# Kernel optimization log

Hardware: AMD Instinct MI355X
Metric: run time of the kernel (lower is better)

## Reference

```python
import jax, jax.numpy as jnp
import numpy as np


def _lsa(cost):
    """Jonker-Volgenant shortest-augmenting-path LAP (same optimum as
    scipy.optimize.linear_sum_assignment). cost: (n, m) with n <= m.
    Returns col4row: (n,) assigned column for each row."""
    cost = np.asarray(cost, dtype=np.float64)
    n, m = cost.shape
    u = np.zeros(n)
    v = np.zeros(m)
    col4row = np.full(n, -1, dtype=np.int64)
    row4col = np.full(m, -1, dtype=np.int64)
    for cur_row in range(n):
        shortest = np.full(m, np.inf)
        path = np.full(m, -1, dtype=np.int64)
        SR = np.zeros(n, dtype=bool)
        SC = np.zeros(m, dtype=bool)
        i = cur_row
        min_val = 0.0
        sink = -1
        while sink == -1:
            SR[i] = True
            rem = np.where(~SC)[0]
            d = min_val + cost[i, rem] - u[i] - v[rem]
            better = d < shortest[rem]
            shortest[rem[better]] = d[better]
            path[rem[better]] = i
            k = rem[np.argmin(shortest[rem])]
            min_val = shortest[k]
            SC[k] = True
            if row4col[k] == -1:
                sink = k
            else:
                i = row4col[k]
        u[cur_row] += min_val
        upd = SR.copy()
        upd[cur_row] = False
        u[upd] += min_val - shortest[col4row[upd]]
        v[SC] -= min_val - shortest[SC]
        j = sink
        while True:
            i = path[j]
            row4col[j] = i
            col4row[i], j = j, col4row[i]
            if i == cur_row:
                break
    return col4row


def _hungarian(cost_np):
    """Mimic scipy.linear_sum_assignment for any (N, M)."""
    n, m = cost_np.shape
    if n <= m:
        col4row = _lsa(cost_np)
        return np.arange(n, dtype=np.int64), col4row
    else:
        row4col = _lsa(cost_np.T)  # for each col of cost, its assigned row
        return row4col, np.arange(m, dtype=np.int64)


def setup_inputs() -> dict:
    key = jax.random.key(0)
    k1, k2 = jax.random.split(key)
    N, M, P = 1024, 1024, 20
    pred_points = jax.random.normal(k1, (N, P, 2), dtype=jnp.float32)
    gt_points = jax.random.normal(k2, (M, P, 2), dtype=jnp.float32)
    return {"pred_points": pred_points, "gt_points": gt_points}


def reference(pred_points, gt_points):
    N = pred_points.shape[0]
    M = gt_points.shape[0]
    if N == 0 or M == 0:
        return pred_points, jnp.zeros((N, 1), dtype=pred_points.dtype)

    # Fused pairwise cost: mean over points of per-point Euclidean distance.
    diff = pred_points[:, None, :, :] - gt_points[None, :, :, :]  # (N, M, P, 2)
    cost = jnp.sqrt(jnp.sum(diff * diff, axis=-1)).mean(axis=-1)  # (N, M)

    row_ind, col_ind = _hungarian(np.asarray(cost))
    row_ind = jnp.asarray(row_ind)
    col_ind = jnp.asarray(col_ind)

    if N <= M:
        matched = jnp.zeros_like(pred_points)
    else:
        matched = pred_points
    matched = matched.at[row_ind].set(gt_points[col_ind])

    conf = jnp.zeros((N,), dtype=cost.dtype)
    conf = conf.at[row_ind].set(jnp.exp(-cost[row_ind, col_ind]))
    return matched, conf[:, None]
```

## Files before the change

kernel.cpp:

```cpp
#include <hip/hip_runtime.h>
#include <math.h>

#define NN 1024
#define PP 20
#define LPC 16
#define SCALE_D 33554432.0
#define INV_SCALE_F (1.0f / 33554432.0f)
#define IMAX 0x7fffffff
#define ARR_CAP 4096

__device__ __forceinline__ float cost_ij(const float* __restrict__ a,
                                         const float* __restrict__ b) {
#pragma clang fp contract(off)
  float s = 0.0f;
#pragma unroll
  for (int p = 0; p < PP; ++p) {
    float dx = a[2 * p]     - b[2 * p];
    float dy = a[2 * p + 1] - b[2 * p + 1];
    s += sqrtf(dx * dx + dy * dy);
  }
  return s / 20.0f;
}

__global__ void cost_kernel(const float* __restrict__ pred,
                            const float* __restrict__ gt,
                            int* __restrict__ ci) {
  int id = blockIdx.x * blockDim.x + threadIdx.x;
  int i = id >> 10;
  int j = id & (NN - 1);
  float c = cost_ij(pred + i * 40, gt + j * 40);
  ci[id] = (int)((double)c * SCALE_D);
}

__global__ void colmin_kernel(const int* __restrict__ ci,
                              int* __restrict__ colv,
                              int* __restrict__ colr) {
  int j = blockIdx.x * blockDim.x + threadIdx.x;
  int mv = ci[j];
  int mi = 0;
#pragma unroll 8
  for (int i = 1; i < NN; ++i) {
    int c = ci[i * NN + j];
    if (c < mv) { mv = c; mi = i; }
  }
  colv[j] = mv;
  colr[j] = mi;
}

__global__ __launch_bounds__(64) void rowmin_kernel(
    const int* __restrict__ ci, const int* __restrict__ colv,
    int* __restrict__ rm1, int* __restrict__ rm2, int* __restrict__ rj1) {
  const int row = blockIdx.x;
  const int lane = threadIdx.x;
  const int* cr = ci + (size_t)row * NN + lane * LPC;
  const int* vr = colv + lane * LPC;
  int4 ca = ((const int4*)cr)[0], cb = ((const int4*)cr)[1],
       cc = ((const int4*)cr)[2], cd = ((const int4*)cr)[3];
  int4 va = ((const int4*)vr)[0], vb = ((const int4*)vr)[1],
       vc = ((const int4*)vr)[2], vd = ((const int4*)vr)[3];
  int c[LPC] = {ca.x, ca.y, ca.z, ca.w, cb.x, cb.y, cb.z, cb.w,
                cc.x, cc.y, cc.z, cc.w, cd.x, cd.y, cd.z, cd.w};
  int v[LPC] = {va.x, va.y, va.z, va.w, vb.x, vb.y, vb.z, vb.w,
                vc.x, vc.y, vc.z, vc.w, vd.x, vd.y, vd.z, vd.w};
  int m1 = IMAX, m2 = IMAX, c1 = IMAX;
#pragma unroll
  for (int q = 0; q < LPC; ++q) {
    const int d = c[q] - v[q];
    if (d < m1) { m2 = m1; m1 = d; c1 = lane * LPC + q; }
    else if (d < m2) m2 = d;
  }
#pragma unroll
  for (int m = 1; m < 64; m <<= 1) {
    const int pm1 = __shfl_xor(m1, m);
    const int pm2 = __shfl_xor(m2, m);
    const int pc1 = __shfl_xor(c1, m);
    const int hi = (m1 > pm1) ? m1 : pm1;
    const int lo2 = (m2 < pm2) ? m2 : pm2;
    if (pm1 < m1 || (pm1 == m1 && pc1 < c1)) { m1 = pm1; c1 = pc1; }
    m2 = (hi < lo2) ? hi : lo2;
  }
  if (lane == 0) { rm1[row] = m1; rm2[row] = m2; rj1[row] = c1; }
}

__device__ __forceinline__ int wave_min_bcast(int x) {
  int t;
  t = __builtin_amdgcn_update_dpp(IMAX, x, 0x111, 0xf, 0xf, false);
  x = (t < x) ? t : x;
  t = __builtin_amdgcn_update_dpp(IMAX, x, 0x112, 0xf, 0xf, false);
  x = (t < x) ? t : x;
  t = __builtin_amdgcn_update_dpp(IMAX, x, 0x114, 0xf, 0xf, false);
  x = (t < x) ? t : x;
  t = __builtin_amdgcn_update_dpp(IMAX, x, 0x118, 0xf, 0xf, false);
  x = (t < x) ? t : x;
  t = __builtin_amdgcn_update_dpp(IMAX, x, 0x142, 0xf, 0xf, false);
  x = (t < x) ? t : x;
  t = __builtin_amdgcn_update_dpp(IMAX, x, 0x143, 0xf, 0xf, false);
  x = (t < x) ? t : x;
  return __builtin_amdgcn_readlane(x, 63);
}

__global__ __launch_bounds__(64) void lap_kernel(
    const float* __restrict__ gt, const int* __restrict__ ci,
    const int* __restrict__ colv, const int* __restrict__ colr,
    const int* __restrict__ rm1, const int* __restrict__ rm2,
    const int* __restrict__ rj1, float* __restrict__ out) {
  const int lane = threadIdx.x;

  __shared__ int u_s[NN];
  __shared__ int row4col_s[NN];
  __shared__ int col4row_s[NN];
  __shared__ int path_s[NN];
  __shared__ int queue_s[NN + ARR_CAP];

  int nv_r[LPC];
  int sh_r[LPC];
  int kq_r[LPC];
  int pa_r[LPC];
  int rc_r[LPC];

  {
    const int4* p4 = (const int4*)ci;
    int ax = 0, ay = 0, az = 0, aw = 0;
    for (int it = 0; it < (NN * NN / 4) / 64; it += 8) {
#pragma unroll
      for (int uu = 0; uu < 8; ++uu) {
        const int4 tv = p4[(size_t)(it + uu) * 64 + lane];
        ax ^= tv.x; ay ^= tv.y; az ^= tv.z; aw ^= tv.w;
      }
    }
    asm volatile("" :: "v"(ax), "v"(ay), "v"(az), "v"(aw));
  }

#pragma unroll
  for (int q = 0; q < LPC; ++q) {
    const int j = lane * LPC + q;
    u_s[j] = 0;
    row4col_s[j] = -1;
    col4row_s[j] = -1;
  }
  __syncthreads();

  if (lane == 0) {
    for (int j = 0; j < NN; ++j) {
      const int i = colr[j];
      if (col4row_s[i] < 0) { col4row_s[i] = j; row4col_s[j] = i; }
    }
  }
  __syncthreads();

#pragma unroll
  for (int q = 0; q < LPC; ++q) {
    const int j = lane * LPC + q;
    const int i = row4col_s[j];
    int nvv = -colv[j];
    if (i >= 0) {
      const int mu = (rj1[i] == j) ? rm2[i] : rm1[i];
      u_s[i] = mu;
      nvv += mu;
    }
    nv_r[q] = nvv;
  }
  if (lane == 0) {
    int n = 0;
    for (int i = 0; i < NN; ++i)
      if (col4row_s[i] < 0) queue_s[n++] = i;
    path_s[0] = n;
  }
  __syncthreads();
  int head = 0;
  int tail = path_s[0];
  __syncthreads();

  for (int step = 0; step < ARR_CAP && head < tail; ++step) {
    const int i = queue_s[head];
    ++head;
    const int* cr = ci + (size_t)i * NN + lane * LPC;
    int4 ca = ((const int4*)cr)[0], cb = ((const int4*)cr)[1],
         cc = ((const int4*)cr)[2], cd = ((const int4*)cr)[3];
    int c[LPC] = {ca.x, ca.y, ca.z, ca.w, cb.x, cb.y, cb.z, cb.w,
                  cc.x, cc.y, cc.z, cc.w, cd.x, cd.y, cd.z, cd.w};
    int m1 = IMAX, m2 = IMAX, c1 = 0;
#pragma unroll
    for (int q = 0; q < LPC; ++q) {
      const int d = c[q] + nv_r[q];
      if (d < m1) { m2 = m1; m1 = d; c1 = q; }
      else if (d < m2) m2 = d;
    }
    const int m1g = wave_min_bcast(m1);
    const unsigned long long ball = __ballot(m1 == m1g);
    const int wl = __ffsll(ball) - 1;
    const int cand = (lane == wl) ? m2 : m1;
    const int m2g = wave_min_bcast(cand);
    const int j1 = (wl << 4) | __builtin_amdgcn_readlane(c1, wl);
    const int delta = m2g - m1g;
    if (lane == wl && delta > 0) {
#pragma unroll
      for (int q = 0; q < LPC; ++q)
        if (q == (j1 & 15)) nv_r[q] += delta;
    }
    const int k = row4col_s[j1];
    __syncthreads();
    if (lane == 0) {
      u_s[i] = m2g;
      row4col_s[j1] = i;
      col4row_s[i] = j1;
      if (k >= 0) {
        col4row_s[k] = -1;
        queue_s[tail] = k;
      }
    }
    if (k >= 0) ++tail;
    __syncthreads();
  }

#pragma unroll
  for (int q = 0; q < LPC; ++q) rc_r[q] = row4col_s[lane * LPC + q];
  __syncthreads();

  const int nfree = tail - head;
  for (int fi = 0; fi < nfree; ++fi) {
    const int r = queue_s[head + fi];
#pragma unroll
    for (int q = 0; q < LPC; ++q) { sh_r[q] = IMAX; kq_r[q] = IMAX; }
    int i = r;
    int mv = 0;
    int A = __builtin_amdgcn_readfirstlane(-u_s[r]);
    int sink;
    while (true) {
      const int* cr = ci + (size_t)i * NN + lane * LPC;
      int4 ca = ((const int4*)cr)[0], cb = ((const int4*)cr)[1],
           cc = ((const int4*)cr)[2], cd = ((const int4*)cr)[3];
      int c[LPC] = {ca.x, ca.y, ca.z, ca.w, cb.x, cb.y, cb.z, cb.w,
                    cc.x, cc.y, cc.z, cc.w, cd.x, cd.y, cd.z, cd.w};
#pragma unroll
      for (int q = 0; q < LPC; ++q) {
        const int d = A + c[q] + nv_r[q];
        const bool upd = d < sh_r[q];
        sh_r[q] = upd ? d : sh_r[q];
        kq_r[q] = upd ? d : kq_r[q];
        pa_r[q] = upd ? i : pa_r[q];
      }
      int t1k[8], t1e[8], t1r[8];
#pragma unroll
      for (int q = 0; q < 8; ++q) {
        const bool b = kq_r[2 * q + 1] < kq_r[2 * q];
        t1k[q] = b ? kq_r[2 * q + 1] : kq_r[2 * q];
        t1e[q] = b ? 2 * q + 1 : 2 * q;
        t1r[q] = b ? rc_r[2 * q + 1] : rc_r[2 * q];
      }
      int t2k[4], t2e[4], t2r[4];
#pragma unroll
      for (int q = 0; q < 4; ++q) {
        const bool b = t1k[2 * q + 1] < t1k[2 * q];
        t2k[q] = b ? t1k[2 * q + 1] : t1k[2 * q];
        t2e[q] = b ? t1e[2 * q + 1] : t1e[2 * q];
        t2r[q] = b ? t1r[2 * q + 1] : t1r[2 * q];
      }
      int t3k[2], t3e[2], t3r[2];
#pragma unroll
      for (int q = 0; q < 2; ++q) {
        const bool b = t2k[2 * q + 1] < t2k[2 * q];
        t3k[q] = b ? t2k[2 * q + 1] : t2k[2 * q];
        t3e[q] = b ? t2e[2 * q + 1] : t2e[2 * q];
        t3r[q] = b ? t2r[2 * q + 1] : t2r[2 * q];
      }
      const bool b0 = t3k[1] < t3k[0];
      const int bs = b0 ? t3k[1] : t3k[0];
      const int bq = b0 ? t3e[1] : t3e[0];
      const int brc = b0 ? t3r[1] : t3r[0];
      const int minkey = wave_min_bcast(bs);
      const unsigned long long ball = __ballot(bs == minkey);
      const int wl = __ffsll(ball) - 1;
      const int kcol = (wl << 4) | __builtin_amdgcn_readlane(bq, wl);
      const int krc = __builtin_amdgcn_readlane(brc, wl);
      mv = minkey;
      if (krc < 0) { sink = kcol; break; }
      if (lane == (kcol >> 4)) {
#pragma unroll
        for (int q = 0; q < LPC; ++q)
          if (q == (kcol & 15)) kq_r[q] = IMAX;
      }
      i = krc;
      A = __builtin_amdgcn_readfirstlane(mv - u_s[i]);
    }
#pragma unroll
    for (int q = 0; q < LPC; ++q) {
      if (kq_r[q] == IMAX && sh_r[q] != IMAX) {
        const int delta = mv - sh_r[q];
        const int i2 = rc_r[q];
        if (i2 >= 0) u_s[i2] += delta;
        nv_r[q] += delta;
      }
      path_s[lane * LPC + q] = pa_r[q];
    }
    if (lane == 0) u_s[r] += mv;
    __syncthreads();
    if (lane == 0) {
      int j = sink;
      while (true) {
        const int i2 = path_s[j];
        row4col_s[j] = i2;
        const int jn = col4row_s[i2];
        col4row_s[i2] = j;
        j = jn;
        if (i2 == r) break;
      }
    }
    __syncthreads();
#pragma unroll
    for (int q = 0; q < LPC; ++q) rc_r[q] = row4col_s[lane * LPC + q];
  }
  __syncthreads();

#pragma unroll
  for (int q = 0; q < LPC; ++q) {
    const int row = lane * LPC + q;
    const int col = col4row_s[row];
    const float4* g4 = (const float4*)(gt + (size_t)col * 40);
    float4* o4 = (float4*)(out + (size_t)row * 40);
#pragma unroll
    for (int w = 0; w < 10; ++w) o4[w] = g4[w];
    const float cf = (float)ci[(size_t)row * NN + col] * INV_SCALE_F;
    out[NN * 40 + row] = expf(-cf);
  }
}

extern "C" void kernel_launch(void* const* d_in, const int* in_sizes, int n_in,
                              void* d_out, int out_size, void* d_ws,
                              size_t ws_size, hipStream_t stream) {
  const float* pred = (const float*)d_in[0];
  const float* gt = (const float*)d_in[1];
  float* out = (float*)d_out;
  int* ci = (int*)d_ws;

  int* colv = (int*)out;
  int* colr = colv + NN;
  int* rm1 = colr + NN;
  int* rm2 = rm1 + NN;
  int* rj1 = rm2 + NN;

  cost_kernel<<<NN * NN / 256, 256, 0, stream>>>(pred, gt, ci);
  colmin_kernel<<<NN / 256, 256, 0, stream>>>(ci, colv, colr);
  rowmin_kernel<<<NN, 64, 0, stream>>>(ci, colv, rm1, rm2, rj1);
  lap_kernel<<<1, 64, 0, stream>>>(gt, ci, colv, colr, rm1, rm2, rj1, out);
}
```

Baseline: 9.874 ms.

## Prefetch next cost row and fuse argmin payload into DPP reductions

```diff
diff --git a/kernel.cpp b/kernel.cpp
--- a/kernel.cpp
+++ b/kernel.cpp
@@ -82,22 +82,68 @@
   if (lane == 0) { rm1[row] = m1; rm2[row] = m2; rj1[row] = c1; }
 }
 
-__device__ __forceinline__ int wave_min_bcast(int x) {
-  int t;
-  t = __builtin_amdgcn_update_dpp(IMAX, x, 0x111, 0xf, 0xf, false);
-  x = (t < x) ? t : x;
-  t = __builtin_amdgcn_update_dpp(IMAX, x, 0x112, 0xf, 0xf, false);
-  x = (t < x) ? t : x;
-  t = __builtin_amdgcn_update_dpp(IMAX, x, 0x114, 0xf, 0xf, false);
-  x = (t < x) ? t : x;
-  t = __builtin_amdgcn_update_dpp(IMAX, x, 0x118, 0xf, 0xf, false);
-  x = (t < x) ? t : x;
-  t = __builtin_amdgcn_update_dpp(IMAX, x, 0x142, 0xf, 0xf, false);
-  x = (t < x) ? t : x;
-  t = __builtin_amdgcn_update_dpp(IMAX, x, 0x143, 0xf, 0xf, false);
-  x = (t < x) ? t : x;
-  return __builtin_amdgcn_readlane(x, 63);
-}
+template <int CTRL>
+__device__ __forceinline__ void argmin_step(int& k, int& p) {
+  const int k2 = __builtin_amdgcn_update_dpp(IMAX, k, CTRL, 0xf, 0xf, false);
+  const int p2 = __builtin_amdgcn_update_dpp(0, p, CTRL, 0xf, 0xf, false);
+  if (k2 < k) { k = k2; p = p2; }
+}
+__device__ __forceinline__ void wave_argmin(int& k, int& p) {
+  argmin_step<0x111>(k, p);
+  argmin_step<0x112>(k, p);
+  argmin_step<0x114>(k, p);
+  argmin_step<0x118>(k, p);
+  argmin_step<0x142>(k, p);
+  argmin_step<0x143>(k, p);
+}
+template <int CTRL>
+__device__ __forceinline__ void top2_step(int& m1, int& m2, int& p1) {
+  const int a1 = __builtin_amdgcn_update_dpp(IMAX, m1, CTRL, 0xf, 0xf, false);
+  const int a2 = __builtin_amdgcn_update_dpp(IMAX, m2, CTRL, 0xf, 0xf, false);
+  const int ap = __builtin_amdgcn_update_dpp(0, p1, CTRL, 0xf, 0xf, false);
+  const int hi = m1 > a1 ? m1 : a1;
+  const int lo = m2 < a2 ? m2 : a2;
+  if (a1 < m1) { m1 = a1; p1 = ap; }
+  m2 = hi < lo ? hi : lo;
+}
+__device__ __forceinline__ void wave_top2(int& m1, int& m2, int& p1) {
+  top2_step<0x111>(m1, m2, p1);
+  top2_step<0x112>(m1, m2, p1);
+  top2_step<0x114>(m1, m2, p1);
+  top2_step<0x118>(m1, m2, p1);
+  top2_step<0x142>(m1, m2, p1);
+  top2_step<0x143>(m1, m2, p1);
+}
+
+#define LGKM_BARRIER()                                \
+  do {                                                \
+    asm volatile("s_waitcnt lgkmcnt(0)" ::: "memory"); \
+    __builtin_amdgcn_s_barrier();                     \
+  } while (0)
+
+#define PF_ISSUE(row)                                                    \
+  do {                                                                   \
+    const int4* _pr = (const int4*)(ci + (size_t)(row)*NN + lane * LPC); \
+    P0 = _pr[0]; P1 = _pr[1]; P2 = _pr[2]; P3 = _pr[3];                  \
+  } while (0)
+
+#define UNPACK_P(c)                                      \
+  do {                                                   \
+    c[0] = P0.x; c[1] = P0.y; c[2] = P0.z; c[3] = P0.w;  \
+    c[4] = P1.x; c[5] = P1.y; c[6] = P1.z; c[7] = P1.w;  \
+    c[8] = P2.x; c[9] = P2.y; c[10] = P2.z; c[11] = P2.w; \
+    c[12] = P3.x; c[13] = P3.y; c[14] = P3.z; c[15] = P3.w; \
+  } while (0)
+
+#define LOAD_C(c, row)                                                   \
+  do {                                                                   \
+    const int4* _cr = (const int4*)(ci + (size_t)(row)*NN + lane * LPC); \
+    const int4 _a = _cr[0], _b = _cr[1], _d = _cr[2], _e = _cr[3];       \
+    c[0] = _a.x; c[1] = _a.y; c[2] = _a.z; c[3] = _a.w;                  \
+    c[4] = _b.x; c[5] = _b.y; c[6] = _b.z; c[7] = _b.w;                  \
+    c[8] = _d.x; c[9] = _d.y; c[10] = _d.z; c[11] = _d.w;                \
+    c[12] = _e.x; c[13] = _e.y; c[14] = _e.z; c[15] = _e.w;              \
+  } while (0)
 
 __global__ __launch_bounds__(64) void lap_kernel(
     const float* __restrict__ gt, const int* __restrict__ ci,
@@ -116,7 +162,9 @@
   int sh_r[LPC];
   int kq_r[LPC];
   int pa_r[LPC];
-  int rc_r[LPC];
+  int prc_r[LPC];
+  int4 P0, P1, P2, P3;
+  int pf_row = -1;
 
   {
     const int4* p4 = (const int4*)ci;
@@ -171,14 +219,16 @@
   int tail = path_s[0];
   __syncthreads();
 
+  if (head < tail) { pf_row = queue_s[head]; PF_ISSUE(pf_row); }
   for (int step = 0; step < ARR_CAP && head < tail; ++step) {
     const int i = queue_s[head];
     ++head;
-    const int* cr = ci + (size_t)i * NN + lane * LPC;
-    int4 ca = ((const int4*)cr)[0], cb = ((const int4*)cr)[1],
-         cc = ((const int4*)cr)[2], cd = ((const int4*)cr)[3];
-    int c[LPC] = {ca.x, ca.y, ca.z, ca.w, cb.x, cb.y, cb.z, cb.w,
-                  cc.x, cc.y, cc.z, cc.w, cd.x, cd.y, cd.z, cd.w};
+    int c[LPC];
+    if (i == pf_row) { UNPACK_P(c); }
+    else             { LOAD_C(c, i); }
+    if (head < tail) { pf_row = queue_s[head]; PF_ISSUE(pf_row); }
+    else pf_row = -1;
+
     int m1 = IMAX, m2 = IMAX, c1 = 0;
 #pragma unroll
     for (int q = 0; q < LPC; ++q) {
@@ -186,20 +236,19 @@
       if (d < m1) { m2 = m1; m1 = d; c1 = q; }
       else if (d < m2) m2 = d;
     }
-    const int m1g = wave_min_bcast(m1);
-    const unsigned long long ball = __ballot(m1 == m1g);
-    const int wl = __ffsll(ball) - 1;
-    const int cand = (lane == wl) ? m2 : m1;
-    const int m2g = wave_min_bcast(cand);
-    const int j1 = (wl << 4) | __builtin_amdgcn_readlane(c1, wl);
+    int p1 = (lane << 4) | c1;
+    wave_top2(m1, m2, p1);
+    const int m1g = __builtin_amdgcn_readlane(m1, 63);
+    const int m2g = __builtin_amdgcn_readlane(m2, 63);
+    const int j1 = __builtin_amdgcn_readlane(p1, 63);
     const int delta = m2g - m1g;
-    if (lane == wl && delta > 0) {
+    if (lane == (j1 >> 4) && delta > 0) {
 #pragma unroll
       for (int q = 0; q < LPC; ++q)
         if (q == (j1 & 15)) nv_r[q] += delta;
     }
     const int k = row4col_s[j1];
-    __syncthreads();
+    LGKM_BARRIER();
     if (lane == 0) {
       u_s[i] = m2g;
       row4col_s[j1] = i;
@@ -210,14 +259,19 @@
       }
     }
     if (k >= 0) ++tail;
-    __syncthreads();
-  }
-
-#pragma unroll
-  for (int q = 0; q < LPC; ++q) rc_r[q] = row4col_s[lane * LPC + q];
+    LGKM_BARRIER();
+  }
+
+#pragma unroll
+  for (int q = 0; q < LPC; ++q) {
+    const int rcq = row4col_s[lane * LPC + q];
+    prc_r[q] = ((rcq + 1) << 10) | (lane * LPC + q);
+  }
   __syncthreads();
 
   const int nfree = tail - head;
+  pf_row = -1;
+  if (nfree > 0) { pf_row = queue_s[head]; PF_ISSUE(pf_row); }
   for (int fi = 0; fi < nfree; ++fi) {
     const int r = queue_s[head + fi];
 #pragma unroll
@@ -227,11 +281,10 @@
     int A = __builtin_amdgcn_readfirstlane(-u_s[r]);
     int sink;
     while (true) {
-      const int* cr = ci + (size_t)i * NN + lane * LPC;
-      int4 ca = ((const int4*)cr)[0], cb = ((const int4*)cr)[1],
-           cc = ((const int4*)cr)[2], cd = ((const int4*)cr)[3];
-      int c[LPC] = {ca.x, ca.y, ca.z, ca.w, cb.x, cb.y, cb.z, cb.w,
-                    cc.x, cc.y, cc.z, cc.w, cd.x, cd.y, cd.z, cd.w};
+      int c[LPC];
+      if (i == pf_row) { UNPACK_P(c); }
+      else             { LOAD_C(c, i); }
+      pf_row = -1;
 #pragma unroll
       for (int q = 0; q < LPC; ++q) {
         const int d = A + c[q] + nv_r[q];
@@ -240,40 +293,35 @@
         kq_r[q] = upd ? d : kq_r[q];
         pa_r[q] = upd ? i : pa_r[q];
       }
-      int t1k[8], t1e[8], t1r[8];
+      int a1k[8], a1p[8];
 #pragma unroll
       for (int q = 0; q < 8; ++q) {
         const bool b = kq_r[2 * q + 1] < kq_r[2 * q];
-        t1k[q] = b ? kq_r[2 * q + 1] : kq_r[2 * q];
-        t1e[q] = b ? 2 * q + 1 : 2 * q;
-        t1r[q] = b ? rc_r[2 * q + 1] : rc_r[2 * q];
-      }
-      int t2k[4], t2e[4], t2r[4];
+        a1k[q] = b ? kq_r[2 * q + 1] : kq_r[2 * q];
+        a1p[q] = b ? prc_r[2 * q + 1] : prc_r[2 * q];
+      }
+      int a2k[4], a2p[4];
 #pragma unroll
       for (int q = 0; q < 4; ++q) {
-        const bool b = t1k[2 * q + 1] < t1k[2 * q];
-        t2k[q] = b ? t1k[2 * q + 1] : t1k[2 * q];
-        t2e[q] = b ? t1e[2 * q + 1] : t1e[2 * q];
-        t2r[q] = b ? t1r[2 * q + 1] : t1r[2 * q];
-      }
-      int t3k[2], t3e[2], t3r[2];
+        const bool b = a1k[2 * q + 1] < a1k[2 * q];
+        a2k[q] = b ? a1k[2 * q + 1] : a1k[2 * q];
+        a2p[q] = b ? a1p[2 * q + 1] : a1p[2 * q];
+      }
+      int a3k[2], a3p[2];
 #pragma unroll
       for (int q = 0; q < 2; ++q) {
-        const bool b = t2k[2 * q + 1] < t2k[2 * q];
-        t3k[q] = b ? t2k[2 * q + 1] : t2k[2 * q];
-        t3e[q] = b ? t2e[2 * q + 1] : t2e[2 * q];
-        t3r[q] = b ? t2r[2 * q + 1] : t2r[2 * q];
-      }
-      const bool b0 = t3k[1] < t3k[0];
-      const int bs = b0 ? t3k[1] : t3k[0];
-      const int bq = b0 ? t3e[1] : t3e[0];
-      const int brc = b0 ? t3r[1] : t3r[0];
-      const int minkey = wave_min_bcast(bs);
-      const unsigned long long ball = __ballot(bs == minkey);
-      const int wl = __ffsll(ball) - 1;
-      const int kcol = (wl << 4) | __builtin_amdgcn_readlane(bq, wl);
-      const int krc = __builtin_amdgcn_readlane(brc, wl);
-      mv = minkey;
+        const bool b = a2k[2 * q + 1] < a2k[2 * q];
+        a3k[q] = b ? a2k[2 * q + 1] : a2k[2 * q];
+        a3p[q] = b ? a2p[2 * q + 1] : a2p[2 * q];
+      }
+      const bool b0 = a3k[1] < a3k[0];
+      int bk = b0 ? a3k[1] : a3k[0];
+      int bp = b0 ? a3p[1] : a3p[0];
+      wave_argmin(bk, bp);
+      mv = __builtin_amdgcn_readlane(bk, 63);
+      const int pk = __builtin_amdgcn_readlane(bp, 63);
+      const int kcol = pk & 1023;
+      const int krc = (pk >> 10) - 1;
       if (krc < 0) { sink = kcol; break; }
       if (lane == (kcol >> 4)) {
 #pragma unroll
@@ -283,18 +331,19 @@
       i = krc;
       A = __builtin_amdgcn_readfirstlane(mv - u_s[i]);
     }
+    if (fi + 1 < nfree) { pf_row = queue_s[head + fi + 1]; PF_ISSUE(pf_row); }
 #pragma unroll
     for (int q = 0; q < LPC; ++q) {
       if (kq_r[q] == IMAX && sh_r[q] != IMAX) {
         const int delta = mv - sh_r[q];
-        const int i2 = rc_r[q];
+        const int i2 = (prc_r[q] >> 10) - 1;
         if (i2 >= 0) u_s[i2] += delta;
         nv_r[q] += delta;
       }
       path_s[lane * LPC + q] = pa_r[q];
     }
     if (lane == 0) u_s[r] += mv;
-    __syncthreads();
+    LGKM_BARRIER();
     if (lane == 0) {
       int j = sink;
       while (true) {
@@ -306,9 +355,12 @@
         if (i2 == r) break;
       }
     }
-    __syncthreads();
-#pragma unroll
-    for (int q = 0; q < LPC; ++q) rc_r[q] = row4col_s[lane * LPC + q];
+    LGKM_BARRIER();
+#pragma unroll
+    for (int q = 0; q < LPC; ++q) {
+      const int rcq = row4col_s[lane * LPC + q];
+      prc_r[q] = ((rcq + 1) << 10) | (lane * LPC + q);
+    }
   }
   __syncthreads();
 
```

Result: slower. 14.89 ms (+50.8%).

## Add parallel auction-style bidding rounds to pre-assign rows before serial LAP

Applied to the files above, without the earlier changes.

```diff
diff --git a/kernel.cpp b/kernel.cpp
--- a/kernel.cpp
+++ b/kernel.cpp
@@ -7,7 +7,8 @@
 #define SCALE_D 33554432.0
 #define INV_SCALE_F (1.0f / 33554432.0f)
 #define IMAX 0x7fffffff
-#define ARR_CAP 4096
+#define NROUNDS 20
+#define ARR_CAP2 1536
 
 __device__ __forceinline__ float cost_ij(const float* __restrict__ a,
                                          const float* __restrict__ b) {
@@ -32,40 +33,49 @@
   ci[id] = (int)((double)c * SCALE_D);
 }
 
+__global__ void init_kernel(int* __restrict__ u, int* __restrict__ r4c,
+                            int* __restrict__ c4r,
+                            unsigned long long* __restrict__ bids) {
+  const int t = blockIdx.x * blockDim.x + threadIdx.x;
+  u[t] = 0;
+  r4c[t] = -1;
+  c4r[t] = -1;
+  bids[t] = 0ull;
+}
+
 __global__ void colmin_kernel(const int* __restrict__ ci,
-                              int* __restrict__ colv,
-                              int* __restrict__ colr) {
+                              int* __restrict__ v) {
   int j = blockIdx.x * blockDim.x + threadIdx.x;
   int mv = ci[j];
-  int mi = 0;
 #pragma unroll 8
   for (int i = 1; i < NN; ++i) {
     int c = ci[i * NN + j];
-    if (c < mv) { mv = c; mi = i; }
-  }
-  colv[j] = mv;
-  colr[j] = mi;
-}
-
-__global__ __launch_bounds__(64) void rowmin_kernel(
-    const int* __restrict__ ci, const int* __restrict__ colv,
-    int* __restrict__ rm1, int* __restrict__ rm2, int* __restrict__ rj1) {
+    if (c < mv) mv = c;
+  }
+  v[j] = mv;
+}
+
+__global__ __launch_bounds__(64) void bid_kernel(
+    const int* __restrict__ ci, const int* __restrict__ v,
+    const int* __restrict__ c4r, int* __restrict__ bidm2,
+    unsigned long long* __restrict__ bids) {
   const int row = blockIdx.x;
+  if (c4r[row] >= 0) return;
   const int lane = threadIdx.x;
   const int* cr = ci + (size_t)row * NN + lane * LPC;
-  const int* vr = colv + lane * LPC;
+  const int* vr = v + lane * LPC;
   int4 ca = ((const int4*)cr)[0], cb = ((const int4*)cr)[1],
        cc = ((const int4*)cr)[2], cd = ((const int4*)cr)[3];
   int4 va = ((const int4*)vr)[0], vb = ((const int4*)vr)[1],
        vc = ((const int4*)vr)[2], vd = ((const int4*)vr)[3];
   int c[LPC] = {ca.x, ca.y, ca.z, ca.w, cb.x, cb.y, cb.z, cb.w,
                 cc.x, cc.y, cc.z, cc.w, cd.x, cd.y, cd.z, cd.w};
-  int v[LPC] = {va.x, va.y, va.z, va.w, vb.x, vb.y, vb.z, vb.w,
-                vc.x, vc.y, vc.z, vc.w, vd.x, vd.y, vd.z, vd.w};
+  int vv[LPC] = {va.x, va.y, va.z, va.w, vb.x, vb.y, vb.z, vb.w,
+                 vc.x, vc.y, vc.z, vc.w, vd.x, vd.y, vd.z, vd.w};
   int m1 = IMAX, m2 = IMAX, c1 = IMAX;
 #pragma unroll
   for (int q = 0; q < LPC; ++q) {
-    const int d = c[q] - v[q];
+    const int d = c[q] - vv[q];
     if (d < m1) { m2 = m1; m1 = d; c1 = lane * LPC + q; }
     else if (d < m2) m2 = d;
   }
@@ -79,7 +89,32 @@
     if (pm1 < m1 || (pm1 == m1 && pc1 < c1)) { m1 = pm1; c1 = pc1; }
     m2 = (hi < lo2) ? hi : lo2;
   }
-  if (lane == 0) { rm1[row] = m1; rm2[row] = m2; rj1[row] = c1; }
+  if (lane == 0) {
+    bidm2[row] = m2;
+    const unsigned long long pk =
+        ((unsigned long long)(unsigned)(m2 - m1) << 32) |
+        (unsigned long long)(unsigned)(row + 1);
+    atomicMax(&bids[c1], pk);
+  }
+}
+
+__global__ void resolve_kernel(const int* __restrict__ ci, int* __restrict__ v,
+                               int* __restrict__ u, int* __restrict__ r4c,
+                               int* __restrict__ c4r,
+                               const int* __restrict__ bidm2,
+                               unsigned long long* __restrict__ bids) {
+  const int j = blockIdx.x * blockDim.x + threadIdx.x;
+  const unsigned long long b = bids[j];
+  if (b == 0ull) return;
+  bids[j] = 0ull;
+  const int row = (int)(b & 0xffffffffull) - 1;
+  const int m2 = bidm2[row];
+  const int disp = r4c[j];
+  r4c[j] = row;
+  c4r[row] = j;
+  if (disp >= 0) c4r[disp] = -1;
+  v[j] = ci[(size_t)row * NN + j] - m2;
+  u[row] = m2;
 }
 
 __device__ __forceinline__ int wave_min_bcast(int x) {
@@ -101,16 +136,16 @@
 
 __global__ __launch_bounds__(64) void lap_kernel(
     const float* __restrict__ gt, const int* __restrict__ ci,
-    const int* __restrict__ colv, const int* __restrict__ colr,
-    const int* __restrict__ rm1, const int* __restrict__ rm2,
-    const int* __restrict__ rj1, float* __restrict__ out) {
+    const int* __restrict__ v_g, const int* __restrict__ u_g,
+    const int* __restrict__ r4c_g, const int* __restrict__ c4r_g,
+    float* __restrict__ out) {
   const int lane = threadIdx.x;
 
   __shared__ int u_s[NN];
   __shared__ int row4col_s[NN];
   __shared__ int col4row_s[NN];
   __shared__ int path_s[NN];
-  __shared__ int queue_s[NN + ARR_CAP];
+  __shared__ int queue_s[NN + ARR_CAP2];
 
   int nv_r[LPC];
   int sh_r[LPC];
@@ -119,12 +154,13 @@
   int rc_r[LPC];
 
   {
-    const int4* p4 = (const int4*)ci;
+    const char* base = (const char*)ci;
     int ax = 0, ay = 0, az = 0, aw = 0;
-    for (int it = 0; it < (NN * NN / 4) / 64; it += 8) {
+    for (int it = 0; it < 1024; it += 8) {
 #pragma unroll
       for (int uu = 0; uu < 8; ++uu) {
-        const int4 tv = p4[(size_t)(it + uu) * 64 + lane];
+        const int4 tv =
+            *(const int4*)(base + ((size_t)(it + uu) * 64 + lane) * 64);
         ax ^= tv.x; ay ^= tv.y; az ^= tv.z; aw ^= tv.w;
       }
     }
@@ -134,32 +170,12 @@
 #pragma unroll
   for (int q = 0; q < LPC; ++q) {
     const int j = lane * LPC + q;
-    u_s[j] = 0;
-    row4col_s[j] = -1;
-    col4row_s[j] = -1;
-  }
-  __syncthreads();
-
-  if (lane == 0) {
-    for (int j = 0; j < NN; ++j) {
-      const int i = colr[j];
-      if (col4row_s[i] < 0) { col4row_s[i] = j; row4col_s[j] = i; }
-    }
-  }
-  __syncthreads();
-
-#pragma unroll
-  for (int q = 0; q < LPC; ++q) {
-    const int j = lane * LPC + q;
-    const int i = row4col_s[j];
-    int nvv = -colv[j];
-    if (i >= 0) {
-      const int mu = (rj1[i] == j) ? rm2[i] : rm1[i];
-      u_s[i] = mu;
-      nvv += mu;
-    }
-    nv_r[q] = nvv;
-  }
+    u_s[j] = u_g[j];
+    row4col_s[j] = r4c_g[j];
+    col4row_s[j] = c4r_g[j];
+    nv_r[q] = -v_g[j];
+  }
+  __syncthreads();
   if (lane == 0) {
     int n = 0;
     for (int i = 0; i < NN; ++i)
@@ -171,7 +187,7 @@
   int tail = path_s[0];
   __syncthreads();
 
-  for (int step = 0; step < ARR_CAP && head < tail; ++step) {
+  for (int step = 0; step < ARR_CAP2 && head < tail; ++step) {
     const int i = queue_s[head];
     ++head;
     const int* cr = ci + (size_t)i * NN + lane * LPC;
@@ -333,14 +349,21 @@
   float* out = (float*)d_out;
   int* ci = (int*)d_ws;
 
-  int* colv = (int*)out;
-  int* colr = colv + NN;
-  int* rm1 = colr + NN;
-  int* rm2 = rm1 + NN;
-  int* rj1 = rm2 + NN;
+  int* v_g = (int*)out;
+  int* u_g = (int*)out + NN;
+  int* r4c = (int*)out + 2 * NN;
+  int* c4r = (int*)out + 3 * NN;
+  int* bidm2 = (int*)out + 4 * NN;
+  unsigned long long* bids =
+      (unsigned long long*)((int*)out + 5 * NN);
 
   cost_kernel<<<NN * NN / 256, 256, 0, stream>>>(pred, gt, ci);
-  colmin_kernel<<<NN / 256, 256, 0, stream>>>(ci, colv, colr);
-  rowmin_kernel<<<NN, 64, 0, stream>>>(ci, colv, rm1, rm2, rj1);
-  lap_kernel<<<1, 64, 0, stream>>>(gt, ci, colv, colr, rm1, rm2, rj1, out);
-}
+  init_kernel<<<NN / 256, 256, 0, stream>>>(u_g, r4c, c4r, bids);
+  colmin_kernel<<<NN / 256, 256, 0, stream>>>(ci, v_g);
+  for (int r = 0; r < NROUNDS; ++r) {
+    bid_kernel<<<NN, 64, 0, stream>>>(ci, v_g, c4r, bidm2, bids);
+    resolve_kernel<<<NN / 256, 256, 0, stream>>>(ci, v_g, u_g, r4c, c4r,
+                                                 bidm2, bids);
+  }
+  lap_kernel<<<1, 64, 0, stream>>>(gt, ci, v_g, u_g, r4c, c4r, out);
+}
```

Measured after the change: 10.03 ms. No clear change (+1.5%).
